# Kernel optimization log

Hardware: AMD Instinct MI355X
Metric: run time of the kernel (lower is better)

Reference implementation:

```python
import jax, jax.numpy as jnp
import numpy as np

H = 1024      # hidden_size
NH = 16       # num_heads
HD = H // NH  # head_dim


def setup_inputs() -> dict:
    key = jax.random.key(0)
    ks = jax.random.split(key, 5)
    x = jax.random.normal(ks[0], (2, 2048, H), dtype=jnp.float32)
    # nn.Linear weights are [out, in]; keep that convention
    w_qkv = jax.random.normal(ks[1], (3 * H, H), dtype=jnp.float32) * (1.0 / np.sqrt(H))
    b_qkv = jax.random.normal(ks[2], (3 * H,), dtype=jnp.float32) * 0.01
    w_out = jax.random.normal(ks[3], (H, H), dtype=jnp.float32) * (1.0 / np.sqrt(H))
    b_out = jax.random.normal(ks[4], (H,), dtype=jnp.float32) * 0.01
    return {"x": x, "w_qkv": w_qkv, "b_qkv": b_qkv, "w_out": w_out, "b_out": b_out}


def reference(x, w_qkv, b_qkv, w_out, b_out):
    B, L, _ = x.shape
    scale = HD ** -0.5
    qkv = x @ w_qkv.T + b_qkv                       # [B,L,3H]
    qkv = qkv.reshape(B, L, 3, NH, HD).transpose(2, 0, 3, 1, 4)  # [3,B,NH,L,HD]
    q, k, v = qkv[0], qkv[1], qkv[2]
    attn = jnp.einsum('bhqd,bhkd->bhqk', q, k) * scale
    attn = jax.nn.softmax(attn, axis=-1)            # dropout is identity in eval
    out = jnp.einsum('bhqk,bhkd->bhqd', attn, v)    # [B,NH,L,HD]
    out = out.transpose(0, 2, 1, 3).reshape(B, L, H)
    return out @ w_out.T + b_out
```

## Files before the change

### kernel.cpp

```cpp
#include <hip/hip_runtime.h>
#include <hip/hip_bf16.h>
#include <stdint.h>

#define H_DIM  1024
#define NHEADS 16
#define HDIM   64
#define BATCH  2
#define SEQ    2048
#define MROWS  (BATCH * SEQ)
#define QKV_N  (3 * H_DIM)
#define QK_LD  (2 * H_DIM)
#define NT     (SEQ / 64)

typedef __attribute__((ext_vector_type(8))) __bf16 bf16x8;
typedef __attribute__((ext_vector_type(4))) float  floatx4;

__device__ __forceinline__ unsigned short f2bf(float f) {
    uint32_t u = __float_as_uint(f);
    u += 0x7fffu + ((u >> 16) & 1u);
    return (unsigned short)(u >> 16);
}
__device__ __forceinline__ float bf2f(unsigned short u) {
    return __uint_as_float(((uint32_t)u) << 16);
}
__device__ __forceinline__ uint32_t cvtpk_bf16(float lo, float hi) {
    uint32_t r;
    asm("v_cvt_pk_bf16_f32 %0, %1, %2" : "=v"(r) : "v"(lo), "v"(hi));
    return r;
}

#if __has_builtin(__builtin_amdgcn_exp2f)
#define fexp2 __builtin_amdgcn_exp2f
#else
#define fexp2 exp2f
#endif

__device__ __forceinline__ void async_ld16(const void* g, void* l) {
    __builtin_amdgcn_global_load_lds(
        (const __attribute__((address_space(1))) void*)g,
        (__attribute__((address_space(3))) void*)l, 16, 0, 0);
}

#define N4_X   (MROWS * H_DIM / 4)
#define N4_WQ  (QKV_N * H_DIM / 4)
#define N4_WO  (H_DIM * H_DIM / 4)
__global__ __launch_bounds__(256) void cvt_all(const float4* __restrict__ x,
                                               const float4* __restrict__ wq,
                                               const float4* __restrict__ wo,
                                               ushort4* __restrict__ xb,
                                               ushort4* __restrict__ wqb,
                                               ushort4* __restrict__ wob) {
    int i = blockIdx.x * 256 + threadIdx.x;
    const float4* in;
    ushort4* out;
    int j;
    if (i < N4_X)                { in = x;  out = xb;  j = i; }
    else if (i < N4_X + N4_WQ)   { in = wq; out = wqb; j = i - N4_X; }
    else                         { in = wo; out = wob; j = i - N4_X - N4_WQ; }
    float4 v = in[j];
    ushort4 o;
    o.x = f2bf(v.x); o.y = f2bf(v.y); o.z = f2bf(v.z); o.w = f2bf(v.w);
    out[j] = o;
}

__global__ __launch_bounds__(256) void transpose_v(const unsigned short* __restrict__ vr,
                                                   unsigned short* __restrict__ vt) {
    __shared__ unsigned short T[64][72];
    const int tid = threadIdx.x;
    const int bh = blockIdx.y;
    const int b = bh >> 4, h = bh & 15;
    const int kv0 = blockIdx.x * 64;
    const int r  = tid >> 2, cs = (tid & 3) * 16;

    const unsigned short* src = &vr[(size_t)(b * SEQ + kv0 + r) * H_DIM + h * HDIM + cs];
    union { uint4 q; unsigned short u[8]; } A0, A1;
    A0.q = *(const uint4*)&src[0];
    A1.q = *(const uint4*)&src[8];
    #pragma unroll
    for (int e = 0; e < 8; ++e) T[cs + e][r]     = A0.u[e];
    #pragma unroll
    for (int e = 0; e < 8; ++e) T[cs + 8 + e][r] = A1.u[e];
    __syncthreads();

    const int dd = tid >> 2, ks = (tid & 3) * 16;
    unsigned short* dst = &vt[((size_t)bh * HDIM + dd) * SEQ + kv0 + ks];
    *(uint4*)&dst[0] = *(const uint4*)&T[dd][ks];
    *(uint4*)&dst[8] = *(const uint4*)&T[dd][ks + 8];
}

__global__ __launch_bounds__(256) void gemm_bt(const unsigned short* __restrict__ A,
                                               const unsigned short* __restrict__ B,
                                               const float* __restrict__ bias,
                                               unsigned short* __restrict__ Cb,
                                               float* __restrict__ Cf,
                                               unsigned short* __restrict__ Vr,
                                               int ldc, int Kdim) {
    __shared__ __align__(16) unsigned short As[128 * 64];
    __shared__ __align__(16) unsigned short Bs[128 * 64];
    const int tid  = threadIdx.x;
    const int lane = tid & 63;
    const int wave = tid >> 6;
    const int waveM = (wave >> 1) * 64;
    const int waveN = (wave & 1) * 64;

    const int nwg = gridDim.x * gridDim.y;
    int wg = blockIdx.y * gridDim.x + blockIdx.x;
    wg = (wg & 7) * (nwg >> 3) + (wg >> 3);
    const int bm = wg / gridDim.x, bn = wg % gridDim.x;

    floatx4 acc[4][4];
    #pragma unroll
    for (int i = 0; i < 4; ++i)
        #pragma unroll
        for (int j = 0; j < 4; ++j) {
            floatx4 z = {0.f, 0.f, 0.f, 0.f};
            acc[i][j] = z;
        }

    int rr[4], kc[4];
    #pragma unroll
    for (int i = 0; i < 4; ++i) {
        int c = i * 256 + tid;
        rr[i] = c >> 3;
        kc[i] = ((c & 7) ^ (rr[i] & 7)) * 8;
    }

    const int lr = lane & 15;
    const int g  = lane >> 4;
    const int sw = lr & 7;

    for (int k0 = 0; k0 < Kdim; k0 += 64) {
        #pragma unroll
        for (int i = 0; i < 4; ++i) {
            async_ld16(&A[(size_t)(bm * 128 + rr[i]) * Kdim + k0 + kc[i]],
                       (char*)As + i * 4096 + wave * 1024);
            async_ld16(&B[(size_t)(bn * 128 + rr[i]) * Kdim + k0 + kc[i]],
                       (char*)Bs + i * 4096 + wave * 1024);
        }
        __syncthreads();

        #pragma unroll
        for (int kk = 0; kk < 2; ++kk) {
            const int gk = (((kk << 2) + g) ^ sw) * 8;
            bf16x8 af[4], bfr[4];
            #pragma unroll
            for (int i = 0; i < 4; ++i)
                af[i] = *(const bf16x8*)&As[(waveM + i * 16 + lr) * 64 + gk];
            #pragma unroll
            for (int j = 0; j < 4; ++j)
                bfr[j] = *(const bf16x8*)&Bs[(waveN + j * 16 + lr) * 64 + gk];

            #pragma unroll
            for (int i = 0; i < 4; ++i)
                #pragma unroll
                for (int j = 0; j < 4; ++j)
                    acc[i][j] = __builtin_amdgcn_mfma_f32_16x16x32_bf16(af[i], bfr[j], acc[i][j], 0, 0, 0);
        }
        __syncthreads();
    }

    const int crow0 = bm * 128 + waveM + (lane >> 4) * 4;
    const int ccol0 = bn * 128 + waveN + (lane & 15);
    #pragma unroll
    for (int i = 0; i < 4; ++i)
        #pragma unroll
        for (int j = 0; j < 4; ++j) {
            int col = ccol0 + j * 16;
            float bv = bias[col];
            #pragma unroll
            for (int r = 0; r < 4; ++r) {
                int row = crow0 + i * 16 + r;
                float v = acc[i][j][r] + bv;
                if (Vr && col >= 2 * H_DIM) {
                    Vr[(size_t)row * H_DIM + (col - 2 * H_DIM)] = f2bf(v);
                } else if (Cb) {
                    Cb[(size_t)row * ldc + col] = f2bf(v);
                } else {
                    Cf[(size_t)row * ldc + col] = v;
                }
            }
        }
}

__global__ __launch_bounds__(256) void gemm_bt64(const unsigned short* __restrict__ A,
                                                 const unsigned short* __restrict__ B,
                                                 const float* __restrict__ bias,
                                                 float* __restrict__ Cf,
                                                 int ldc, int Kdim) {
    __shared__ __align__(16) unsigned short As[128 * 64];
    __shared__ __align__(16) unsigned short Bs[64 * 64];
    const int tid  = threadIdx.x;
    const int lane = tid & 63;
    const int wave = tid >> 6;
    const int waveM = wave * 32;

    const int nwg = gridDim.x * gridDim.y;
    int wg = blockIdx.y * gridDim.x + blockIdx.x;
    wg = (wg & 7) * (nwg >> 3) + (wg >> 3);
    const int bm = wg / gridDim.x, bn = wg % gridDim.x;

    floatx4 acc[2][4];
    #pragma unroll
    for (int i = 0; i < 2; ++i)
        #pragma unroll
        for (int j = 0; j < 4; ++j) {
            floatx4 z = {0.f, 0.f, 0.f, 0.f};
            acc[i][j] = z;
        }

    int rr[4], kc[4];
    #pragma unroll
    for (int i = 0; i < 4; ++i) {
        int c = i * 256 + tid;
        rr[i] = c >> 3;
        kc[i] = ((c & 7) ^ (rr[i] & 7)) * 8;
    }

    const int lr = lane & 15;
    const int g  = lane >> 4;
    const int sw = lr & 7;

    for (int k0 = 0; k0 < Kdim; k0 += 64) {
        #pragma unroll
        for (int i = 0; i < 4; ++i)
            async_ld16(&A[(size_t)(bm * 128 + rr[i]) * Kdim + k0 + kc[i]],
                       (char*)As + i * 4096 + wave * 1024);
        #pragma unroll
        for (int i = 0; i < 2; ++i)
            async_ld16(&B[(size_t)(bn * 64 + rr[i]) * Kdim + k0 + kc[i]],
                       (char*)Bs + i * 4096 + wave * 1024);
        __syncthreads();

        #pragma unroll
        for (int kk = 0; kk < 2; ++kk) {
            const int gk = (((kk << 2) + g) ^ sw) * 8;
            bf16x8 af[2], bfr[4];
            #pragma unroll
            for (int i = 0; i < 2; ++i)
                af[i] = *(const bf16x8*)&As[(waveM + i * 16 + lr) * 64 + gk];
            #pragma unroll
            for (int j = 0; j < 4; ++j)
                bfr[j] = *(const bf16x8*)&Bs[(j * 16 + lr) * 64 + gk];

            #pragma unroll
            for (int i = 0; i < 2; ++i)
                #pragma unroll
                for (int j = 0; j < 4; ++j)
                    acc[i][j] = __builtin_amdgcn_mfma_f32_16x16x32_bf16(af[i], bfr[j], acc[i][j], 0, 0, 0);
        }
        __syncthreads();
    }

    const int crow0 = bm * 128 + waveM + (lane >> 4) * 4;
    const int ccol0 = bn * 64 + (lane & 15);
    #pragma unroll
    for (int i = 0; i < 2; ++i)
        #pragma unroll
        for (int j = 0; j < 4; ++j) {
            int col = ccol0 + j * 16;
            float bv = bias[col];
            #pragma unroll
            for (int r = 0; r < 4; ++r) {
                int row = crow0 + i * 16 + r;
                Cf[(size_t)row * ldc + col] = acc[i][j][r] + bv;
            }
        }
}

__global__ __launch_bounds__(256, 2) void attn_mfma(const unsigned short* __restrict__ qkv2,
                                                    const unsigned short* __restrict__ vt,
                                                    unsigned short* __restrict__ ctx) {
    __shared__ __align__(16) unsigned short Ks2[2][64 * 64];
    __shared__ __align__(16) unsigned short Vt2[2][64 * 64];

    const int tid  = threadIdx.x;
    const int lane = tid & 63;
    const int wave = tid >> 6;

    const int f  = blockIdx.y * gridDim.x + blockIdx.x;
    const int bh = ((f >> 7) << 3) + (f & 7);
    const int qt = (f >> 3) & 15;
    const int b  = bh >> 4, h = bh & 15;
    const int q0 = qt * 128 + wave * 32;
    const int lq = lane & 15;
    const int g  = lane >> 4;
    const int swz = lq & 7;

    const float QS = 0.125f * 1.44269504f;
    bf16x8 qf[2][2];
    #pragma unroll
    for (int s = 0; s < 2; ++s)
        #pragma unroll
        for (int kk = 0; kk < 2; ++kk) {
            union { bf16x8 v; unsigned short u[8]; } tq;
            tq.v = *(const bf16x8*)&qkv2[(size_t)(b * SEQ + q0 + s * 16 + lq) * QK_LD
                                         + h * HDIM + kk * 32 + g * 8];
            #pragma unroll
            for (int e = 0; e < 8; ++e) tq.u[e] = f2bf(bf2f(tq.u[e]) * QS);
            qf[s][kk] = tq.v;
        }

    floatx4 acc_o[2][4];
    #pragma unroll
    for (int s = 0; s < 2; ++s)
        #pragma unroll
        for (int j = 0; j < 4; ++j) {
            floatx4 z = {0.f, 0.f, 0.f, 0.f};
            acc_o[s][j] = z;
        }
    float l_run[2] = {0.f, 0.f};

    const unsigned short* gK = qkv2 + (size_t)b * SEQ * QK_LD + H_DIM + (size_t)h * HDIM;
    const unsigned short* gV = vt + (size_t)bh * HDIM * SEQ;

    const int r0  = tid >> 3;
    const int pr0 = (r0 & 32) | ((r0 & 12) << 1) | ((r0 & 16) >> 2) | (r0 & 3);
    const int gs0 = (tid & 7) ^ (r0 & 7);
    const unsigned short* pK0 = gK + (size_t)pr0 * QK_LD + gs0 * 8;
    const unsigned short* pK1 = gK + (size_t)(pr0 + 32) * QK_LD + gs0 * 8;
    const unsigned short* pV0 = gV + (size_t)r0 * SEQ + gs0 * 8;
    const unsigned short* pV1 = gV + (size_t)(r0 + 32) * SEQ + gs0 * 8;

    #define STAGE_KV(bi)                                                        \
        {                                                                       \
            async_ld16(pK0, (char*)&Ks2[bi][0] + (wave * 64) * 16);             \
            async_ld16(pK1, (char*)&Ks2[bi][0] + (256 + wave * 64) * 16);       \
            async_ld16(pV0, (char*)&Vt2[bi][0] + (wave * 64) * 16);             \
            async_ld16(pV1, (char*)&Vt2[bi][0] + (256 + wave * 64) * 16);       \
            pK0 += 64 * QK_LD; pK1 += 64 * QK_LD; pV0 += 64; pV1 += 64;         \
        }

    STAGE_KV(0)
    __syncthreads();

    int buf = 0;
    for (int t = 0; t < NT; ++t) {
        if (t + 1 < NT) STAGE_KV(buf ^ 1)

        const unsigned short* Ksb = &Ks2[buf][0];
        const unsigned short* Vsb = &Vt2[buf][0];

        bf16x8 kf[4][2];
        #pragma unroll
        for (int jb = 0; jb < 4; ++jb)
            #pragma unroll
            for (int kk = 0; kk < 2; ++kk)
                kf[jb][kk] = *(const bf16x8*)&Ksb[(jb * 16 + lq) * 64 + (((kk << 2) + g) ^ swz) * 8];

        bf16x8 vf[4][2];
        #pragma unroll
        for (int dt = 0; dt < 4; ++dt)
            #pragma unroll
            for (int kk = 0; kk < 2; ++kk)
                vf[dt][kk] = *(const bf16x8*)&Vsb[(dt * 16 + lq) * 64 + (((kk << 2) + g) ^ swz) * 8];

        __builtin_amdgcn_sched_barrier(0);

        floatx4 sa[2][4];
        #pragma unroll
        for (int s = 0; s < 2; ++s)
            #pragma unroll
            for (int jb = 0; jb < 4; ++jb) {
                floatx4 z = {0.f, 0.f, 0.f, 0.f};
                sa[s][jb] = z;
            }
        __builtin_amdgcn_s_setprio(1);
        #pragma unroll
        for (int s = 0; s < 2; ++s)
            #pragma unroll
            for (int jb = 0; jb < 4; ++jb)
                #pragma unroll
                for (int kk = 0; kk < 2; ++kk)
                    sa[s][jb] = __builtin_amdgcn_mfma_f32_16x16x32_bf16(kf[jb][kk], qf[s][kk], sa[s][jb], 0, 0, 0);
        __builtin_amdgcn_s_setprio(0);

        #pragma unroll
        for (int s = 0; s < 2; ++s) {
            float ps = 0.f;
            {
                float e00 = fexp2(sa[s][0][0]), e01 = fexp2(sa[s][0][1]), e02 = fexp2(sa[s][0][2]), e03 = fexp2(sa[s][0][3]);
                float e10 = fexp2(sa[s][1][0]), e11 = fexp2(sa[s][1][1]), e12 = fexp2(sa[s][1][2]), e13 = fexp2(sa[s][1][3]);
                ps += ((e00 + e01) + (e02 + e03)) + ((e10 + e11) + (e12 + e13));
                union { bf16x8 v; uint32_t u[4]; } pf;
                pf.u[0] = cvtpk_bf16(e00, e01); pf.u[1] = cvtpk_bf16(e02, e03);
                pf.u[2] = cvtpk_bf16(e10, e11); pf.u[3] = cvtpk_bf16(e12, e13);
                __builtin_amdgcn_s_setprio(1);
                #pragma unroll
                for (int dt = 0; dt < 4; ++dt)
                    acc_o[s][dt] = __builtin_amdgcn_mfma_f32_16x16x32_bf16(pf.v, vf[dt][0], acc_o[s][dt], 0, 0, 0);
                __builtin_amdgcn_s_setprio(0);
            }
            {
                float e00 = fexp2(sa[s][2][0]), e01 = fexp2(sa[s][2][1]), e02 = fexp2(sa[s][2][2]), e03 = fexp2(sa[s][2][3]);
                float e10 = fexp2(sa[s][3][0]), e11 = fexp2(sa[s][3][1]), e12 = fexp2(sa[s][3][2]), e13 = fexp2(sa[s][3][3]);
                ps += ((e00 + e01) + (e02 + e03)) + ((e10 + e11) + (e12 + e13));
                union { bf16x8 v; uint32_t u[4]; } pf;
                pf.u[0] = cvtpk_bf16(e00, e01); pf.u[1] = cvtpk_bf16(e02, e03);
                pf.u[2] = cvtpk_bf16(e10, e11); pf.u[3] = cvtpk_bf16(e12, e13);
                __builtin_amdgcn_s_setprio(1);
                #pragma unroll
                for (int dt = 0; dt < 4; ++dt)
                    acc_o[s][dt] = __builtin_amdgcn_mfma_f32_16x16x32_bf16(pf.v, vf[dt][1], acc_o[s][dt], 0, 0, 0);
                __builtin_amdgcn_s_setprio(0);
            }
            ps += __shfl_xor(ps, 16);
            ps += __shfl_xor(ps, 32);
            l_run[s] += ps;
        }

        __syncthreads();
        buf ^= 1;
    }
    #undef STAGE_KV

    #pragma unroll
    for (int s = 0; s < 2; ++s) {
        float linv[4];
        #pragma unroll
        for (int r = 0; r < 4; ++r)
            linv[r] = 1.f / __shfl(l_run[s], g * 4 + r);
        #pragma unroll
        for (int dt = 0; dt < 4; ++dt)
            #pragma unroll
            for (int r = 0; r < 4; ++r)
                ctx[(size_t)(b * SEQ + q0 + s * 16 + g * 4 + r) * H_DIM + h * HDIM + dt * 16 + lq]
                    = f2bf(acc_o[s][dt][r] * linv[r]);
    }
}

extern "C" void kernel_launch(void* const* d_in, const int* in_sizes, int n_in,
                              void* d_out, int out_size, void* d_ws, size_t ws_size,
                              hipStream_t stream) {
    const float* x     = (const float*)d_in[0];
    const float* w_qkv = (const float*)d_in[1];
    const float* b_qkv = (const float*)d_in[2];
    const float* w_out = (const float*)d_in[3];
    const float* b_out = (const float*)d_in[4];
    float* out = (float*)d_out;

    unsigned short* xb    = (unsigned short*)d_ws;
    unsigned short* wqkvb = xb    + (size_t)MROWS * H_DIM;
    unsigned short* woutb = wqkvb + (size_t)QKV_N * H_DIM;
    unsigned short* qkv2  = woutb + (size_t)H_DIM * H_DIM;
    unsigned short* ctxb  = qkv2  + (size_t)MROWS * QK_LD;
    unsigned short* vtb   = ctxb  + (size_t)MROWS * H_DIM;
    unsigned short* vrows = ctxb;

    cvt_all<<<(N4_X + N4_WQ + N4_WO) / 256, 256, 0, stream>>>(
        (const float4*)x, (const float4*)w_qkv, (const float4*)w_out,
        (ushort4*)xb, (ushort4*)wqkvb, (ushort4*)woutb);

    gemm_bt<<<dim3(QKV_N / 128, MROWS / 128), 256, 0, stream>>>(xb, wqkvb, b_qkv, qkv2, nullptr, vrows, QK_LD, H_DIM);

    transpose_v<<<dim3(SEQ / 64, BATCH * NHEADS), 256, 0, stream>>>(vrows, vtb);

    attn_mfma<<<dim3(SEQ / 128, BATCH * NHEADS), 256, 0, stream>>>(qkv2, vtb, ctxb);

    gemm_bt64<<<dim3(H_DIM / 64, MROWS / 128), 256, 0, stream>>>(ctxb, woutb, b_out, out, H_DIM, H_DIM);
}
```

Measured before the change: 187.5 us.

## Fuse V transpose into QKV GEMM epilogue and double-buffer output GEMM

The QKV GEMM epilogue now stages V-column tiles through reused shared memory and writes them directly in the transposed [b,h,d,seq] layout, so the separate transpose_v kernel and its extra global round-trip go away. The output projection GEMM also gets double-buffered LDS staging that prefetches the next K tile while the current one is computed. In exchange, the epilogue is more complex and the second GEMM uses twice the LDS, which may lower occupancy.

```diff
diff --git a/kernel.cpp b/kernel.cpp
--- a/kernel.cpp
+++ b/kernel.cpp
@@ -63,37 +63,12 @@
     out[j] = o;
 }
 
-__global__ __launch_bounds__(256) void transpose_v(const unsigned short* __restrict__ vr,
-                                                   unsigned short* __restrict__ vt) {
-    __shared__ unsigned short T[64][72];
-    const int tid = threadIdx.x;
-    const int bh = blockIdx.y;
-    const int b = bh >> 4, h = bh & 15;
-    const int kv0 = blockIdx.x * 64;
-    const int r  = tid >> 2, cs = (tid & 3) * 16;
-
-    const unsigned short* src = &vr[(size_t)(b * SEQ + kv0 + r) * H_DIM + h * HDIM + cs];
-    union { uint4 q; unsigned short u[8]; } A0, A1;
-    A0.q = *(const uint4*)&src[0];
-    A1.q = *(const uint4*)&src[8];
-    #pragma unroll
-    for (int e = 0; e < 8; ++e) T[cs + e][r]     = A0.u[e];
-    #pragma unroll
-    for (int e = 0; e < 8; ++e) T[cs + 8 + e][r] = A1.u[e];
-    __syncthreads();
-
-    const int dd = tid >> 2, ks = (tid & 3) * 16;
-    unsigned short* dst = &vt[((size_t)bh * HDIM + dd) * SEQ + kv0 + ks];
-    *(uint4*)&dst[0] = *(const uint4*)&T[dd][ks];
-    *(uint4*)&dst[8] = *(const uint4*)&T[dd][ks + 8];
-}
-
 __global__ __launch_bounds__(256) void gemm_bt(const unsigned short* __restrict__ A,
                                                const unsigned short* __restrict__ B,
                                                const float* __restrict__ bias,
                                                unsigned short* __restrict__ Cb,
                                                float* __restrict__ Cf,
-                                               unsigned short* __restrict__ Vr,
+                                               unsigned short* __restrict__ Vt,
                                                int ldc, int Kdim) {
     __shared__ __align__(16) unsigned short As[128 * 64];
     __shared__ __align__(16) unsigned short Bs[128 * 64];
@@ -159,27 +134,51 @@
         __syncthreads();
     }
 
-    const int crow0 = bm * 128 + waveM + (lane >> 4) * 4;
-    const int ccol0 = bn * 128 + waveN + (lane & 15);
-    #pragma unroll
-    for (int i = 0; i < 4; ++i)
+    if (Vt && bn >= 16) {
+        unsigned short* Tw = (wave < 2 ? (unsigned short*)As : (unsigned short*)Bs)
+                             + (wave & 1) * 4096;
         #pragma unroll
         for (int j = 0; j < 4; ++j) {
-            int col = ccol0 + j * 16;
-            float bv = bias[col];
-            #pragma unroll
-            for (int r = 0; r < 4; ++r) {
-                int row = crow0 + i * 16 + r;
-                float v = acc[i][j][r] + bv;
-                if (Vr && col >= 2 * H_DIM) {
-                    Vr[(size_t)row * H_DIM + (col - 2 * H_DIM)] = f2bf(v);
-                } else if (Cb) {
-                    Cb[(size_t)row * ldc + col] = f2bf(v);
-                } else {
-                    Cf[(size_t)row * ldc + col] = v;
+            const int n  = j * 16 + lr;
+            const float bv = bias[bn * 128 + waveN + n];
+            #pragma unroll
+            for (int i = 0; i < 4; ++i) {
+                ushort4 pk;
+                pk.x = f2bf(acc[i][j][0] + bv);
+                pk.y = f2bf(acc[i][j][1] + bv);
+                pk.z = f2bf(acc[i][j][2] + bv);
+                pk.w = f2bf(acc[i][j][3] + bv);
+                const int gm = 2 * i + (g >> 1);
+                *(ushort4*)&Tw[n * 64 + (((gm) ^ (n & 7)) << 3) + ((g & 1) << 2)] = pk;
+            }
+        }
+        const int colg = bn * 128 + waveN + lane;
+        const int hd = colg - 2 * H_DIM;
+        const int hh = hd >> 6, dd = hd & 63;
+        const int kvb = bm * 128 + waveM;
+        const int bb = kvb >> 11, kv0 = kvb & (SEQ - 1);
+        unsigned short* dst = &Vt[((size_t)((bb << 4) + hh) * HDIM + dd) * SEQ + kv0];
+        #pragma unroll
+        for (int c = 0; c < 8; ++c)
+            *(uint4*)&dst[c * 8] = *(const uint4*)&Tw[lane * 64 + ((c ^ (lane & 7)) << 3)];
+    } else {
+        const int crow0 = bm * 128 + waveM + (lane >> 4) * 4;
+        const int ccol0 = bn * 128 + waveN + (lane & 15);
+        #pragma unroll
+        for (int i = 0; i < 4; ++i)
+            #pragma unroll
+            for (int j = 0; j < 4; ++j) {
+                int col = ccol0 + j * 16;
+                float bv = bias[col];
+                #pragma unroll
+                for (int r = 0; r < 4; ++r) {
+                    int row = crow0 + i * 16 + r;
+                    float v = acc[i][j][r] + bv;
+                    if (Cb) Cb[(size_t)row * ldc + col] = f2bf(v);
+                    else    Cf[(size_t)row * ldc + col] = v;
                 }
             }
-        }
+    }
 }
 
 __global__ __launch_bounds__(256) void gemm_bt64(const unsigned short* __restrict__ A,
@@ -187,8 +186,8 @@
                                                  const float* __restrict__ bias,
                                                  float* __restrict__ Cf,
                                                  int ldc, int Kdim) {
-    __shared__ __align__(16) unsigned short As[128 * 64];
-    __shared__ __align__(16) unsigned short Bs[64 * 64];
+    __shared__ __align__(16) unsigned short As2[2][128 * 64];
+    __shared__ __align__(16) unsigned short Bs2[2][64 * 64];
     const int tid  = threadIdx.x;
     const int lane = tid & 63;
     const int wave = tid >> 6;
@@ -220,16 +219,25 @@
     const int g  = lane >> 4;
     const int sw = lr & 7;
 
-    for (int k0 = 0; k0 < Kdim; k0 += 64) {
-        #pragma unroll
-        for (int i = 0; i < 4; ++i)
-            async_ld16(&A[(size_t)(bm * 128 + rr[i]) * Kdim + k0 + kc[i]],
-                       (char*)As + i * 4096 + wave * 1024);
-        #pragma unroll
-        for (int i = 0; i < 2; ++i)
-            async_ld16(&B[(size_t)(bn * 64 + rr[i]) * Kdim + k0 + kc[i]],
-                       (char*)Bs + i * 4096 + wave * 1024);
-        __syncthreads();
+    #define STAGE64(bi, k0)                                                          \
+        {                                                                            \
+            _Pragma("unroll")                                                        \
+            for (int i = 0; i < 4; ++i)                                              \
+                async_ld16(&A[(size_t)(bm * 128 + rr[i]) * Kdim + (k0) + kc[i]],     \
+                           (char*)As2[bi] + i * 4096 + wave * 1024);                 \
+            _Pragma("unroll")                                                        \
+            for (int i = 0; i < 2; ++i)                                              \
+                async_ld16(&B[(size_t)(bn * 64 + rr[i]) * Kdim + (k0) + kc[i]],      \
+                           (char*)Bs2[bi] + i * 4096 + wave * 1024);                 \
+        }
+
+    STAGE64(0, 0)
+    __syncthreads();
+
+    int buf = 0;
+    const int nit = Kdim / 64;
+    for (int it = 0; it < nit; ++it) {
+        if (it + 1 < nit) STAGE64(buf ^ 1, (it + 1) * 64)
 
         #pragma unroll
         for (int kk = 0; kk < 2; ++kk) {
@@ -237,10 +245,10 @@
             bf16x8 af[2], bfr[4];
             #pragma unroll
             for (int i = 0; i < 2; ++i)
-                af[i] = *(const bf16x8*)&As[(waveM + i * 16 + lr) * 64 + gk];
+                af[i] = *(const bf16x8*)&As2[buf][(waveM + i * 16 + lr) * 64 + gk];
             #pragma unroll
             for (int j = 0; j < 4; ++j)
-                bfr[j] = *(const bf16x8*)&Bs[(j * 16 + lr) * 64 + gk];
+                bfr[j] = *(const bf16x8*)&Bs2[buf][(j * 16 + lr) * 64 + gk];
 
             #pragma unroll
             for (int i = 0; i < 2; ++i)
@@ -249,7 +257,9 @@
                     acc[i][j] = __builtin_amdgcn_mfma_f32_16x16x32_bf16(af[i], bfr[j], acc[i][j], 0, 0, 0);
         }
         __syncthreads();
-    }
+        buf ^= 1;
+    }
+    #undef STAGE64
 
     const int crow0 = bm * 128 + waveM + (lane >> 4) * 4;
     const int ccol0 = bn * 64 + (lane & 15);
@@ -444,15 +454,12 @@
     unsigned short* qkv2  = woutb + (size_t)H_DIM * H_DIM;
     unsigned short* ctxb  = qkv2  + (size_t)MROWS * QK_LD;
     unsigned short* vtb   = ctxb  + (size_t)MROWS * H_DIM;
-    unsigned short* vrows = ctxb;
 
     cvt_all<<<(N4_X + N4_WQ + N4_WO) / 256, 256, 0, stream>>>(
         (const float4*)x, (const float4*)w_qkv, (const float4*)w_out,
         (ushort4*)xb, (ushort4*)wqkvb, (ushort4*)woutb);
 
-    gemm_bt<<<dim3(QKV_N / 128, MROWS / 128), 256, 0, stream>>>(xb, wqkvb, b_qkv, qkv2, nullptr, vrows, QK_LD, H_DIM);
-
-    transpose_v<<<dim3(SEQ / 64, BATCH * NHEADS), 256, 0, stream>>>(vrows, vtb);
+    gemm_bt<<<dim3(QKV_N / 128, MROWS / 128), 256, 0, stream>>>(xb, wqkvb, b_qkv, qkv2, nullptr, vtb, QK_LD, H_DIM);
 
     attn_mfma<<<dim3(SEQ / 128, BATCH * NHEADS), 256, 0, stream>>>(qkv2, vtb, ctxb);
 
```

Result: slower. 191.9 us (+2.4%).

## Double-buffer LDS tiles in both GEMM kernels to overlap loads with MFMA

Applied to the files above, without the earlier changes.

Both projection GEMMs now use two LDS buffers and prefetch the next K-tile with async loads before computing on the current one. They wait only on the older batch of loads via explicit vmcnt counts, then issue raw s_barrier. The aim is to hide global-memory latency behind the MFMA work. LDS use doubles (64KB for the QKV GEMM), which may lower occupancy, and the hand-set vmcnt values must match the number of issued loads or the results are wrong.

```diff
diff --git a/kernel.cpp b/kernel.cpp
--- a/kernel.cpp
+++ b/kernel.cpp
@@ -95,8 +95,8 @@
                                                float* __restrict__ Cf,
                                                unsigned short* __restrict__ Vr,
                                                int ldc, int Kdim) {
-    __shared__ __align__(16) unsigned short As[128 * 64];
-    __shared__ __align__(16) unsigned short Bs[128 * 64];
+    __shared__ __align__(16) unsigned short As2[2][128 * 64];
+    __shared__ __align__(16) unsigned short Bs2[2][128 * 64];
     const int tid  = threadIdx.x;
     const int lane = tid & 63;
     const int wave = tid >> 6;
@@ -129,15 +129,28 @@
     const int g  = lane >> 4;
     const int sw = lr & 7;
 
+    #define STAGEG(bi, k0)                                                          \
+        {                                                                           \
+            _Pragma("unroll")                                                       \
+            for (int i = 0; i < 4; ++i) {                                           \
+                async_ld16(&A[(size_t)(bm * 128 + rr[i]) * Kdim + (k0) + kc[i]],    \
+                           (char*)As2[bi] + i * 4096 + wave * 1024);                \
+                async_ld16(&B[(size_t)(bn * 128 + rr[i]) * Kdim + (k0) + kc[i]],    \
+                           (char*)Bs2[bi] + i * 4096 + wave * 1024);                \
+            }                                                                       \
+        }
+
+    STAGEG(0, 0)
+
+    int buf = 0;
     for (int k0 = 0; k0 < Kdim; k0 += 64) {
-        #pragma unroll
-        for (int i = 0; i < 4; ++i) {
-            async_ld16(&A[(size_t)(bm * 128 + rr[i]) * Kdim + k0 + kc[i]],
-                       (char*)As + i * 4096 + wave * 1024);
-            async_ld16(&B[(size_t)(bn * 128 + rr[i]) * Kdim + k0 + kc[i]],
-                       (char*)Bs + i * 4096 + wave * 1024);
-        }
-        __syncthreads();
+        if (k0 + 64 < Kdim) {
+            STAGEG(buf ^ 1, k0 + 64)
+            asm volatile("s_waitcnt vmcnt(8)" ::: "memory");
+        } else {
+            asm volatile("s_waitcnt vmcnt(0)" ::: "memory");
+        }
+        __builtin_amdgcn_s_barrier();
 
         #pragma unroll
         for (int kk = 0; kk < 2; ++kk) {
@@ -145,10 +158,10 @@
             bf16x8 af[4], bfr[4];
             #pragma unroll
             for (int i = 0; i < 4; ++i)
-                af[i] = *(const bf16x8*)&As[(waveM + i * 16 + lr) * 64 + gk];
+                af[i] = *(const bf16x8*)&As2[buf][(waveM + i * 16 + lr) * 64 + gk];
             #pragma unroll
             for (int j = 0; j < 4; ++j)
-                bfr[j] = *(const bf16x8*)&Bs[(waveN + j * 16 + lr) * 64 + gk];
+                bfr[j] = *(const bf16x8*)&Bs2[buf][(waveN + j * 16 + lr) * 64 + gk];
 
             #pragma unroll
             for (int i = 0; i < 4; ++i)
@@ -156,8 +169,10 @@
                 for (int j = 0; j < 4; ++j)
                     acc[i][j] = __builtin_amdgcn_mfma_f32_16x16x32_bf16(af[i], bfr[j], acc[i][j], 0, 0, 0);
         }
-        __syncthreads();
-    }
+        __builtin_amdgcn_s_barrier();
+        buf ^= 1;
+    }
+    #undef STAGEG
 
     const int crow0 = bm * 128 + waveM + (lane >> 4) * 4;
     const int ccol0 = bn * 128 + waveN + (lane & 15);
@@ -187,8 +202,8 @@
                                                  const float* __restrict__ bias,
                                                  float* __restrict__ Cf,
                                                  int ldc, int Kdim) {
-    __shared__ __align__(16) unsigned short As[128 * 64];
-    __shared__ __align__(16) unsigned short Bs[64 * 64];
+    __shared__ __align__(16) unsigned short As2[2][128 * 64];
+    __shared__ __align__(16) unsigned short Bs2[2][64 * 64];
     const int tid  = threadIdx.x;
     const int lane = tid & 63;
     const int wave = tid >> 6;
@@ -220,16 +235,29 @@
     const int g  = lane >> 4;
     const int sw = lr & 7;
 
+    #define STAGE64(bi, k0)                                                          \
+        {                                                                            \
+            _Pragma("unroll")                                                        \
+            for (int i = 0; i < 4; ++i)                                              \
+                async_ld16(&A[(size_t)(bm * 128 + rr[i]) * Kdim + (k0) + kc[i]],     \
+                           (char*)As2[bi] + i * 4096 + wave * 1024);                 \
+            _Pragma("unroll")                                                        \
+            for (int i = 0; i < 2; ++i)                                              \
+                async_ld16(&B[(size_t)(bn * 64 + rr[i]) * Kdim + (k0) + kc[i]],      \
+                           (char*)Bs2[bi] + i * 4096 + wave * 1024);                 \
+        }
+
+    STAGE64(0, 0)
+
+    int buf = 0;
     for (int k0 = 0; k0 < Kdim; k0 += 64) {
-        #pragma unroll
-        for (int i = 0; i < 4; ++i)
-            async_ld16(&A[(size_t)(bm * 128 + rr[i]) * Kdim + k0 + kc[i]],
-                       (char*)As + i * 4096 + wave * 1024);
-        #pragma unroll
-        for (int i = 0; i < 2; ++i)
-            async_ld16(&B[(size_t)(bn * 64 + rr[i]) * Kdim + k0 + kc[i]],
-                       (char*)Bs + i * 4096 + wave * 1024);
-        __syncthreads();
+        if (k0 + 64 < Kdim) {
+            STAGE64(buf ^ 1, k0 + 64)
+            asm volatile("s_waitcnt vmcnt(6)" ::: "memory");
+        } else {
+            asm volatile("s_waitcnt vmcnt(0)" ::: "memory");
+        }
+        __builtin_amdgcn_s_barrier();
 
         #pragma unroll
         for (int kk = 0; kk < 2; ++kk) {
@@ -237,10 +265,10 @@
             bf16x8 af[2], bfr[4];
             #pragma unroll
             for (int i = 0; i < 2; ++i)
-                af[i] = *(const bf16x8*)&As[(waveM + i * 16 + lr) * 64 + gk];
+                af[i] = *(const bf16x8*)&As2[buf][(waveM + i * 16 + lr) * 64 + gk];
             #pragma unroll
             for (int j = 0; j < 4; ++j)
-                bfr[j] = *(const bf16x8*)&Bs[(j * 16 + lr) * 64 + gk];
+                bfr[j] = *(const bf16x8*)&Bs2[buf][(j * 16 + lr) * 64 + gk];
 
             #pragma unroll
             for (int i = 0; i < 2; ++i)
@@ -248,8 +276,10 @@
                 for (int j = 0; j < 4; ++j)
                     acc[i][j] = __builtin_amdgcn_mfma_f32_16x16x32_bf16(af[i], bfr[j], acc[i][j], 0, 0, 0);
         }
-        __syncthreads();
-    }
+        __builtin_amdgcn_s_barrier();
+        buf ^= 1;
+    }
+    #undef STAGE64
 
     const int crow0 = bm * 128 + waveM + (lane >> 4) * 4;
     const int ccol0 = bn * 64 + (lane & 15);
@@ -450,11 +480,13 @@
         (const float4*)x, (const float4*)w_qkv, (const float4*)w_out,
         (ushort4*)xb, (ushort4*)wqkvb, (ushort4*)woutb);
 
-    gemm_bt<<<dim3(QKV_N / 128, MROWS / 128), 256, 0, stream>>>(xb, wqkvb, b_qkv, qkv2, nullptr, vrows, QK_LD, H_DIM);
+    gemm_bt<<<dim3(QKV_N / 128, MROWS / 128), 256, 0, stream>>>(
+        xb, wqkvb, b_qkv, qkv2, nullptr, vrows, QK_LD, H_DIM);
 
     transpose_v<<<dim3(SEQ / 64, BATCH * NHEADS), 256, 0, stream>>>(vrows, vtb);
 
     attn_mfma<<<dim3(SEQ / 128, BATCH * NHEADS), 256, 0, stream>>>(qkv2, vtb, ctxb);
 
-    gemm_bt64<<<dim3(H_DIM / 64, MROWS / 128), 256, 0, stream>>>(ctxb, woutb, b_out, out, H_DIM, H_DIM);
-}
+    gemm_bt64<<<dim3(H_DIM / 64, MROWS / 128), 256, 0, stream>>>(
+        ctxb, woutb, b_out, out, H_DIM, H_DIM);
+}
```

Measured after the change: 193.8 us. 3.4% more time.
